# Performance work log

Measured on AMD Instinct MI355X. Metric: run time of the kernel, lower is better.

The kernel has to match this reference:

```python
import jax, jax.numpy as jnp
import numpy as np

B, N, D = 131072, 5, 12   # batch, objects per scene, per-object feature dim
E = 64                    # goal embedding / F1 output dim
H = E // 2                # F1 hidden dim = 32


def setup_inputs() -> dict:
    key = jax.random.key(0)
    ks = jax.random.split(key, 6)
    return {
        "obs": jax.random.normal(ks[0], (B, N, D), dtype=jnp.float32),
        "ghat": jax.random.normal(ks[1], (B, E), dtype=jnp.float32),
        "W1": jax.random.normal(ks[2], (2 * D, H), dtype=jnp.float32) * 0.1,
        "b1": jax.random.normal(ks[3], (H,), dtype=jnp.float32) * 0.1,
        "W2": jax.random.normal(ks[4], (H, E), dtype=jnp.float32) * 0.1,
        "b2": jax.random.normal(ks[5], (E,), dtype=jnp.float32) * 0.1,
    }


def reference(obs, ghat, W1, b1, W2, b2):
    b, n, d = obs.shape
    # all-pairs concat: pairs[i,j,k] = cat(obs[i,j], obs[i,k])  -> [B,N,N,2D]
    o_j = jnp.broadcast_to(obs[:, :, None, :], (b, n, n, d))
    o_k = jnp.broadcast_to(obs[:, None, :, :], (b, n, n, d))
    pairs = jnp.concatenate([o_j, o_k], axis=-1)
    # F1 MLP: Linear -> ReLU -> Linear  -> Z [B,N,N,E]
    Z = jnp.maximum(pairs @ W1 + b1, 0.0) @ W2 + b2
    # attention logits w[i,j,k] = <Z[i,j,k], ghat[i]>; softmax over all N*N pairs
    w = jnp.einsum('bjke,be->bjk', Z, ghat)
    p = jax.nn.softmax(w.reshape(b, -1), axis=1).reshape(b, n, n)
    # z_vector[i,j,k] = sum_e p[i,j,k]*Z[i,j,k,e]; zhat[i,j] = sum_k z_vector
    zhat = jnp.einsum('bjk,bjk->bj', p, Z.sum(axis=-1))  # [B,N]
    # state_rep[i,j] = cat(obs[i,j], ghat[i], zhat[i])  -> [B,N,D+E+N]
    state = jnp.concatenate([
        obs,
        jnp.broadcast_to(ghat[:, None, :], (b, n, E)),
        jnp.broadcast_to(zhat[:, None, :], (b, n, n)),
    ], axis=-1)
    return state.reshape(b, -1)  # Flatten -> [B, N*(D+E+N)] = [B, 405]
```

## Files before the change

### kernel.cpp

```cpp
#include <hip/hip_runtime.h>

#define BLOCK 256
#define NB 5
#define DD 12
#define EE 64
#define HH 32
#define ROW 81
#define OUTW 405
#define TILE 64

__global__ __launch_bounds__(BLOCK) void zhat_kernel(
    const float* __restrict__ obs, const float* __restrict__ ghat,
    const float* __restrict__ W1, const float* __restrict__ b1,
    const float* __restrict__ W2, const float* __restrict__ b2,
    float* __restrict__ zbuf, int zstride, int zoff, int B)
{
    __shared__ float s_w2s[HH];
    __shared__ float s_sb2;
    __shared__ float s_g2[BLOCK * 33];

    const int tid = threadIdx.x;

    if (tid < HH) {
        float s = 0.f;
        #pragma unroll
        for (int e = 0; e < EE; ++e) s += W2[tid * EE + e];
        s_w2s[tid] = s;
    } else if (tid == HH) {
        float s = 0.f;
        #pragma unroll
        for (int e = 0; e < EE; ++e) s += b2[e];
        s_sb2 = s;
    }

    const int i = blockIdx.x * BLOCK + tid;

    float g2[HH];
    #pragma unroll
    for (int h = 0; h < HH; ++h) g2[h] = 0.f;
    if (i < B) {
        const float* grow = ghat + (size_t)i * EE;
        #pragma unroll
        for (int e0 = 0; e0 < EE; e0 += 16) {
            float gc[16];
            const float4* gp = reinterpret_cast<const float4*>(grow + e0);
            #pragma unroll
            for (int q = 0; q < 4; ++q) {
                float4 v = gp[q];
                gc[4*q+0] = v.x; gc[4*q+1] = v.y; gc[4*q+2] = v.z; gc[4*q+3] = v.w;
            }
            #pragma unroll
            for (int h = 0; h < HH; ++h) {
                #pragma unroll
                for (int q = 0; q < 16; ++q)
                    g2[h] += W2[h * EE + e0 + q] * gc[q];
            }
        }
    }
    #pragma unroll
    for (int h = 0; h < HH; ++h) s_g2[tid * 33 + h] = g2[h];
    __syncthreads();

    if (i < B) {
        float o[NB * DD];
        {
            const float4* p = reinterpret_cast<const float4*>(obs + (size_t)i * (NB * DD));
            #pragma unroll
            for (int q = 0; q < NB * DD / 4; ++q) {
                float4 v = p[q];
                o[4*q+0] = v.x; o[4*q+1] = v.y; o[4*q+2] = v.z; o[4*q+3] = v.w;
            }
        }

        float w[NB * NB];
        float hw[NB * NB];
        #pragma unroll
        for (int q = 0; q < NB * NB; ++q) { w[q] = 0.f; hw[q] = 0.f; }

        for (int c = 0; c < HH / 8; ++c) {
            float g2c[8], w2c[8];
            #pragma unroll
            for (int hp = 0; hp < 8; ++hp) {
                g2c[hp] = s_g2[tid * 33 + c * 8 + hp];
                w2c[hp] = s_w2s[c * 8 + hp];
            }
            #pragma unroll
            for (int hp = 0; hp < 8; ++hp) {
                const int h = c * 8 + hp;
                float a[NB], bb[NB];
                #pragma unroll
                for (int j = 0; j < NB; ++j) {
                    float acc = b1[h];
                    float accb = 0.f;
                    #pragma unroll
                    for (int d = 0; d < DD; ++d) {
                        acc  += o[j*DD + d] * W1[d*HH + h];
                        accb += o[j*DD + d] * W1[(DD + d)*HH + h];
                    }
                    a[j] = acc; bb[j] = accb;
                }
                #pragma unroll
                for (int j = 0; j < NB; ++j) {
                    #pragma unroll
                    for (int k = 0; k < NB; ++k) {
                        float hv = fmaxf(a[j] + bb[k], 0.f);
                        w[j*NB + k]  += hv * g2c[hp];
                        hw[j*NB + k] += hv * w2c[hp];
                    }
                }
            }
        }

        float m = w[0];
        #pragma unroll
        for (int q = 1; q < NB * NB; ++q) m = fmaxf(m, w[q]);
        float l = 0.f;
        float zacc[NB], racc[NB];
        #pragma unroll
        for (int j = 0; j < NB; ++j) { zacc[j] = 0.f; racc[j] = 0.f; }
        #pragma unroll
        for (int j = 0; j < NB; ++j) {
            #pragma unroll
            for (int k = 0; k < NB; ++k) {
                float e = __expf(w[j*NB + k] - m);
                l += e;
                zacc[j] += e * hw[j*NB + k];
                racc[j] += e;
            }
        }
        const float invl = 1.f / l;
        const float sb2 = s_sb2;
        float* zr = zbuf + (size_t)i * zstride + zoff;
        #pragma unroll
        for (int j = 0; j < NB; ++j)
            zr[j] = (zacc[j] + sb2 * racc[j]) * invl;
    }
}

__global__ __launch_bounds__(BLOCK) void assemble_kernel(
    const float* __restrict__ obs, const float* __restrict__ ghat,
    const float* __restrict__ zbuf, int zstride, int zoff,
    float* __restrict__ out, int B)
{
    __shared__ float s_obs[TILE * NB * DD];
    __shared__ float s_gh[TILE * EE];
    __shared__ float s_zh[TILE * NB];

    const int tid = threadIdx.x;
    const int r0 = blockIdx.x * TILE;
    const int rows = (B - r0 < TILE) ? (B - r0) : TILE;

    for (int t = tid; t < rows * NB * DD; t += BLOCK)
        s_obs[t] = obs[(size_t)r0 * NB * DD + t];
    for (int t = tid; t < rows * EE; t += BLOCK)
        s_gh[t] = ghat[(size_t)r0 * EE + t];
    for (int t = tid; t < rows * NB; t += BLOCK) {
        const int row = t / NB, k = t - row * NB;
        s_zh[t] = zbuf[(size_t)(r0 + row) * zstride + zoff + k];
    }
    __syncthreads();

    const size_t base = (size_t)r0 * OUTW;
    for (int t = tid; t < rows * OUTW; t += BLOCK) {
        const int il = t / OUTW;
        const int r  = t - il * OUTW;
        const int j  = r / ROW;
        const int rr = r - j * ROW;
        float v;
        if (rr < DD)           v = s_obs[il * NB * DD + j * DD + rr];
        else if (rr < DD + EE) v = s_gh[il * EE + (rr - DD)];
        else                   v = s_zh[il * NB + (rr - (DD + EE))];
        out[base + t] = v;
    }
}

extern "C" void kernel_launch(void* const* d_in, const int* in_sizes, int n_in,
                              void* d_out, int out_size, void* d_ws, size_t ws_size,
                              hipStream_t stream) {
    const float* obs  = (const float*)d_in[0];
    const float* ghat = (const float*)d_in[1];
    const float* W1   = (const float*)d_in[2];
    const float* b1   = (const float*)d_in[3];
    const float* W2   = (const float*)d_in[4];
    const float* b2   = (const float*)d_in[5];
    float* out = (float*)d_out;

    const int B = in_sizes[0] / (NB * DD);

    float* zbuf; int zstride, zoff;
    if (ws_size >= (size_t)B * NB * sizeof(float)) {
        zbuf = (float*)d_ws; zstride = NB;   zoff = 0;
    } else {
        zbuf = out;          zstride = OUTW; zoff = OUTW - NB;
    }

    const int gridA = (B + BLOCK - 1) / BLOCK;
    hipLaunchKernelGGL(zhat_kernel, dim3(gridA), dim3(BLOCK), 0, stream,
                       obs, ghat, W1, b1, W2, b2, zbuf, zstride, zoff, B);

    const int gridB = (B + TILE - 1) / TILE;
    hipLaunchKernelGGL(assemble_kernel, dim3(gridB), dim3(BLOCK), 0, stream,
                       obs, ghat, zbuf, zstride, zoff, out, B);
}
```

Baseline: 146.5 us.

## Split hidden dimension across four threads per row with shuffle reductions

The zhat kernel now assigns four threads to each batch row, with each thread handling 8 of the 32 hidden units. Partial logits and z sums are combined with xor shuffles. This drops the large shared g2 buffer and stages a transposed W1 in shared memory. To save registers, the first-layer hidden activations are recomputed in a second pass after the softmax instead of keeping both accumulator arrays. The aim is more parallelism and occupancy, at the cost of duplicated obs loads and repeated W1 arithmetic. An early return follows the only barrier, so there is no sync hazard.

```diff
diff --git a/kernel.cpp b/kernel.cpp
--- a/kernel.cpp
+++ b/kernel.cpp
@@ -8,6 +8,8 @@
 #define ROW 81
 #define OUTW 405
 #define TILE 64
+#define TPB 4
+#define HPT (HH / TPB)
 
 __global__ __launch_bounds__(BLOCK) void zhat_kernel(
     const float* __restrict__ obs, const float* __restrict__ ghat,
@@ -15,119 +17,171 @@
     const float* __restrict__ W2, const float* __restrict__ b2,
     float* __restrict__ zbuf, int zstride, int zoff, int B)
 {
+    __shared__ float s_W1t[HH * 2 * DD];
     __shared__ float s_w2s[HH];
     __shared__ float s_sb2;
-    __shared__ float s_g2[BLOCK * 33];
 
     const int tid = threadIdx.x;
 
     if (tid < HH) {
         float s = 0.f;
-        #pragma unroll
-        for (int e = 0; e < EE; ++e) s += W2[tid * EE + e];
+        const float4* p = reinterpret_cast<const float4*>(W2 + tid * EE);
+        #pragma unroll
+        for (int q = 0; q < EE / 4; ++q) { float4 v = p[q]; s += (v.x + v.y) + (v.z + v.w); }
         s_w2s[tid] = s;
+        #pragma unroll
+        for (int d = 0; d < 2 * DD; ++d) s_W1t[tid * (2 * DD) + d] = W1[d * HH + tid];
     } else if (tid == HH) {
         float s = 0.f;
         #pragma unroll
         for (int e = 0; e < EE; ++e) s += b2[e];
         s_sb2 = s;
     }
-
-    const int i = blockIdx.x * BLOCK + tid;
-
-    float g2[HH];
-    #pragma unroll
-    for (int h = 0; h < HH; ++h) g2[h] = 0.f;
-    if (i < B) {
-        const float* grow = ghat + (size_t)i * EE;
-        #pragma unroll
-        for (int e0 = 0; e0 < EE; e0 += 16) {
-            float gc[16];
-            const float4* gp = reinterpret_cast<const float4*>(grow + e0);
-            #pragma unroll
-            for (int q = 0; q < 4; ++q) {
-                float4 v = gp[q];
-                gc[4*q+0] = v.x; gc[4*q+1] = v.y; gc[4*q+2] = v.z; gc[4*q+3] = v.w;
-            }
-            #pragma unroll
-            for (int h = 0; h < HH; ++h) {
-                #pragma unroll
-                for (int q = 0; q < 16; ++q)
-                    g2[h] += W2[h * EE + e0 + q] * gc[q];
-            }
-        }
-    }
-    #pragma unroll
-    for (int h = 0; h < HH; ++h) s_g2[tid * 33 + h] = g2[h];
     __syncthreads();
 
-    if (i < B) {
-        float o[NB * DD];
-        {
-            const float4* p = reinterpret_cast<const float4*>(obs + (size_t)i * (NB * DD));
-            #pragma unroll
-            for (int q = 0; q < NB * DD / 4; ++q) {
-                float4 v = p[q];
-                o[4*q+0] = v.x; o[4*q+1] = v.y; o[4*q+2] = v.z; o[4*q+3] = v.w;
-            }
-        }
-
-        float w[NB * NB];
-        float hw[NB * NB];
-        #pragma unroll
-        for (int q = 0; q < NB * NB; ++q) { w[q] = 0.f; hw[q] = 0.f; }
-
-        for (int c = 0; c < HH / 8; ++c) {
-            float g2c[8], w2c[8];
-            #pragma unroll
-            for (int hp = 0; hp < 8; ++hp) {
-                g2c[hp] = s_g2[tid * 33 + c * 8 + hp];
-                w2c[hp] = s_w2s[c * 8 + hp];
-            }
-            #pragma unroll
-            for (int hp = 0; hp < 8; ++hp) {
-                const int h = c * 8 + hp;
-                float a[NB], bb[NB];
-                #pragma unroll
-                for (int j = 0; j < NB; ++j) {
-                    float acc = b1[h];
-                    float accb = 0.f;
-                    #pragma unroll
-                    for (int d = 0; d < DD; ++d) {
-                        acc  += o[j*DD + d] * W1[d*HH + h];
-                        accb += o[j*DD + d] * W1[(DD + d)*HH + h];
-                    }
-                    a[j] = acc; bb[j] = accb;
-                }
-                #pragma unroll
-                for (int j = 0; j < NB; ++j) {
-                    #pragma unroll
-                    for (int k = 0; k < NB; ++k) {
-                        float hv = fmaxf(a[j] + bb[k], 0.f);
-                        w[j*NB + k]  += hv * g2c[hp];
-                        hw[j*NB + k] += hv * w2c[hp];
-                    }
-                }
-            }
-        }
-
-        float m = w[0];
-        #pragma unroll
-        for (int q = 1; q < NB * NB; ++q) m = fmaxf(m, w[q]);
-        float l = 0.f;
-        float zacc[NB], racc[NB];
-        #pragma unroll
-        for (int j = 0; j < NB; ++j) { zacc[j] = 0.f; racc[j] = 0.f; }
+    const int g  = tid & (TPB - 1);
+    const int il = tid >> 2;
+    const int i  = blockIdx.x * (BLOCK / TPB) + il;
+    if (i >= B) return;
+
+    float g2[HPT];
+    #pragma unroll
+    for (int hp = 0; hp < HPT; ++hp) g2[hp] = 0.f;
+    const float* grow = ghat + (size_t)i * EE;
+    #pragma unroll 4
+    for (int ec = 0; ec < EE / 4; ++ec) {
+        const float4 gv = reinterpret_cast<const float4*>(grow)[ec];
+        #pragma unroll
+        for (int hp = 0; hp < HPT; ++hp) {
+            const float4 wv = reinterpret_cast<const float4*>(W2 + (g + TPB * hp) * EE)[ec];
+            g2[hp] += gv.x * wv.x + gv.y * wv.y + gv.z * wv.z + gv.w * wv.w;
+        }
+    }
+
+    float o[NB * DD];
+    {
+        const float4* p = reinterpret_cast<const float4*>(obs + (size_t)i * (NB * DD));
+        #pragma unroll
+        for (int q = 0; q < NB * DD / 4; ++q) {
+            float4 v = p[q];
+            o[4*q+0] = v.x; o[4*q+1] = v.y; o[4*q+2] = v.z; o[4*q+3] = v.w;
+        }
+    }
+
+    float w[NB * NB];
+    #pragma unroll
+    for (int q = 0; q < NB * NB; ++q) w[q] = 0.f;
+
+    #pragma unroll
+    for (int hp = 0; hp < HPT; ++hp) {
+        const int h = g + TPB * hp;
+        float a[NB], bb[NB];
+        const float b1h = b1[h];
+        #pragma unroll
+        for (int j = 0; j < NB; ++j) { a[j] = b1h; bb[j] = 0.f; }
+        const float* w1r = &s_W1t[h * (2 * DD)];
+        #pragma unroll
+        for (int dc = 0; dc < 3; ++dc) {
+            const float4 wv = reinterpret_cast<const float4*>(w1r)[dc];
+            const float wl[4] = {wv.x, wv.y, wv.z, wv.w};
+            #pragma unroll
+            for (int d4 = 0; d4 < 4; ++d4) {
+                const int d = dc * 4 + d4;
+                #pragma unroll
+                for (int j = 0; j < NB; ++j) a[j] += o[j*DD + d] * wl[d4];
+            }
+        }
+        #pragma unroll
+        for (int dc = 0; dc < 3; ++dc) {
+            const float4 wv = reinterpret_cast<const float4*>(w1r + DD)[dc];
+            const float wl[4] = {wv.x, wv.y, wv.z, wv.w};
+            #pragma unroll
+            for (int d4 = 0; d4 < 4; ++d4) {
+                const int d = dc * 4 + d4;
+                #pragma unroll
+                for (int j = 0; j < NB; ++j) bb[j] += o[j*DD + d] * wl[d4];
+            }
+        }
+        const float gv = g2[hp];
+        #pragma unroll
+        for (int j = 0; j < NB; ++j)
+            #pragma unroll
+            for (int k = 0; k < NB; ++k)
+                w[j*NB + k] += fmaxf(a[j] + bb[k], 0.f) * gv;
+    }
+
+    #pragma unroll
+    for (int q = 0; q < NB * NB; ++q) {
+        w[q] += __shfl_xor(w[q], 1);
+        w[q] += __shfl_xor(w[q], 2);
+    }
+
+    float m = w[0];
+    #pragma unroll
+    for (int q = 1; q < NB * NB; ++q) m = fmaxf(m, w[q]);
+    #pragma unroll
+    for (int q = 0; q < NB * NB; ++q) w[q] = __expf(w[q] - m);
+    float l = 0.f;
+    float racc[NB];
+    #pragma unroll
+    for (int j = 0; j < NB; ++j) {
+        float r = 0.f;
+        #pragma unroll
+        for (int k = 0; k < NB; ++k) r += w[j*NB + k];
+        racc[j] = r; l += r;
+    }
+
+    float zacc[NB];
+    #pragma unroll
+    for (int j = 0; j < NB; ++j) zacc[j] = 0.f;
+
+    #pragma unroll
+    for (int hp = 0; hp < HPT; ++hp) {
+        const int h = g + TPB * hp;
+        float a[NB], bb[NB];
+        const float b1h = b1[h];
+        #pragma unroll
+        for (int j = 0; j < NB; ++j) { a[j] = b1h; bb[j] = 0.f; }
+        const float* w1r = &s_W1t[h * (2 * DD)];
+        #pragma unroll
+        for (int dc = 0; dc < 3; ++dc) {
+            const float4 wv = reinterpret_cast<const float4*>(w1r)[dc];
+            const float wl[4] = {wv.x, wv.y, wv.z, wv.w};
+            #pragma unroll
+            for (int d4 = 0; d4 < 4; ++d4) {
+                const int d = dc * 4 + d4;
+                #pragma unroll
+                for (int j = 0; j < NB; ++j) a[j] += o[j*DD + d] * wl[d4];
+            }
+        }
+        #pragma unroll
+        for (int dc = 0; dc < 3; ++dc) {
+            const float4 wv = reinterpret_cast<const float4*>(w1r + DD)[dc];
+            const float wl[4] = {wv.x, wv.y, wv.z, wv.w};
+            #pragma unroll
+            for (int d4 = 0; d4 < 4; ++d4) {
+                const int d = dc * 4 + d4;
+                #pragma unroll
+                for (int j = 0; j < NB; ++j) bb[j] += o[j*DD + d] * wl[d4];
+            }
+        }
+        const float ws = s_w2s[h];
         #pragma unroll
         for (int j = 0; j < NB; ++j) {
-            #pragma unroll
-            for (int k = 0; k < NB; ++k) {
-                float e = __expf(w[j*NB + k] - m);
-                l += e;
-                zacc[j] += e * hw[j*NB + k];
-                racc[j] += e;
-            }
-        }
+            float racc2 = 0.f;
+            #pragma unroll
+            for (int k = 0; k < NB; ++k)
+                racc2 += w[j*NB + k] * fmaxf(a[j] + bb[k], 0.f);
+            zacc[j] += ws * racc2;
+        }
+    }
+
+    #pragma unroll
+    for (int j = 0; j < NB; ++j) {
+        zacc[j] += __shfl_xor(zacc[j], 1);
+        zacc[j] += __shfl_xor(zacc[j], 2);
+    }
+    if (g == 0) {
         const float invl = 1.f / l;
         const float sb2 = s_sb2;
         float* zr = zbuf + (size_t)i * zstride + zoff;
@@ -194,7 +248,7 @@
         zbuf = out;          zstride = OUTW; zoff = OUTW - NB;
     }
 
-    const int gridA = (B + BLOCK - 1) / BLOCK;
+    const int gridA = (B + (BLOCK / TPB) - 1) / (BLOCK / TPB);
     hipLaunchKernelGGL(zhat_kernel, dim3(gridA), dim3(BLOCK), 0, stream,
                        obs, ghat, W1, b1, W2, b2, zbuf, zstride, zoff, B);
 
```

After: 321.5 us. 2.19x slower.

## Split hidden units across thread pairs per row and stage W1 in shared memory

Applied to the files above, without the earlier changes.

Each batch row is now handled by two adjacent lanes, each covering half of the 32 hidden units, and the partial attention logits and weighted sums are combined with an xor shuffle before the softmax. W1 is transposed into shared memory and read with float4 loads, and b1 is staged there too. This doubles the thread count and halves the per-thread register load so latency is hidden better. The cost is redundant ghat@W2 work and redundant obs loads in both lanes, plus the shuffle reduction.

```diff
diff --git a/kernel.cpp b/kernel.cpp
--- a/kernel.cpp
+++ b/kernel.cpp
@@ -8,6 +8,8 @@
 #define ROW 81
 #define OUTW 405
 #define TILE 64
+#define BPB 128
+#define W1P 28
 
 __global__ __launch_bounds__(BLOCK) void zhat_kernel(
     const float* __restrict__ obs, const float* __restrict__ ghat,
@@ -15,16 +17,23 @@
     const float* __restrict__ W2, const float* __restrict__ b2,
     float* __restrict__ zbuf, int zstride, int zoff, int B)
 {
+    __shared__ float s_W1t[HH * W1P];
+    __shared__ float s_b1[HH];
     __shared__ float s_w2s[HH];
     __shared__ float s_sb2;
-    __shared__ float s_g2[BLOCK * 33];
+    __shared__ float s_g2[BLOCK * 17];
 
     const int tid = threadIdx.x;
 
     if (tid < HH) {
+        #pragma unroll
+        for (int d = 0; d < 2 * DD; ++d)
+            s_W1t[tid * W1P + d] = W1[d * HH + tid];
+        s_b1[tid] = b1[tid];
         float s = 0.f;
-        #pragma unroll
-        for (int e = 0; e < EE; ++e) s += W2[tid * EE + e];
+        const float4* p = reinterpret_cast<const float4*>(W2 + tid * EE);
+        #pragma unroll
+        for (int q = 0; q < EE / 4; ++q) { float4 v = p[q]; s += (v.x + v.y) + (v.z + v.w); }
         s_w2s[tid] = s;
     } else if (tid == HH) {
         float s = 0.f;
@@ -33,101 +42,120 @@
         s_sb2 = s;
     }
 
-    const int i = blockIdx.x * BLOCK + tid;
-
-    float g2[HH];
-    #pragma unroll
-    for (int h = 0; h < HH; ++h) g2[h] = 0.f;
-    if (i < B) {
+    const int lane = tid & 63;
+    const int par  = lane & 1;
+    const int slot = (tid >> 6) * 32 + (lane >> 1);
+    int i = blockIdx.x * BPB + slot;
+    const bool valid = (i < B);
+    if (!valid) i = (B > 0) ? B - 1 : 0;
+
+    float o[NB * DD];
+    {
+        const float4* p = reinterpret_cast<const float4*>(obs + (size_t)i * (NB * DD));
+        #pragma unroll
+        for (int q = 0; q < NB * DD / 4; ++q) {
+            float4 v = p[q];
+            o[4*q+0] = v.x; o[4*q+1] = v.y; o[4*q+2] = v.z; o[4*q+3] = v.w;
+        }
+    }
+
+    {
+        float g2[HH];
+        #pragma unroll
+        for (int h = 0; h < HH; ++h) g2[h] = 0.f;
         const float* grow = ghat + (size_t)i * EE;
-        #pragma unroll
-        for (int e0 = 0; e0 < EE; e0 += 16) {
-            float gc[16];
-            const float4* gp = reinterpret_cast<const float4*>(grow + e0);
-            #pragma unroll
-            for (int q = 0; q < 4; ++q) {
-                float4 v = gp[q];
-                gc[4*q+0] = v.x; gc[4*q+1] = v.y; gc[4*q+2] = v.z; gc[4*q+3] = v.w;
+        #pragma unroll 1
+        for (int ec = 0; ec < 8; ++ec) {
+            float gc[8];
+            const float4* gp = reinterpret_cast<const float4*>(grow + ec * 8);
+            float4 v0 = gp[0], v1 = gp[1];
+            gc[0]=v0.x; gc[1]=v0.y; gc[2]=v0.z; gc[3]=v0.w;
+            gc[4]=v1.x; gc[5]=v1.y; gc[6]=v1.z; gc[7]=v1.w;
+            #pragma unroll
+            for (int q = 0; q < 8; ++q) {
+                #pragma unroll
+                for (int h = 0; h < HH; ++h)
+                    g2[h] += gc[q] * W2[h * EE + ec * 8 + q];
             }
-            #pragma unroll
-            for (int h = 0; h < HH; ++h) {
+        }
+        if (par == 0) {
+            #pragma unroll
+            for (int hp = 0; hp < 16; ++hp) s_g2[tid * 17 + hp] = g2[hp];
+        } else {
+            #pragma unroll
+            for (int hp = 0; hp < 16; ++hp) s_g2[tid * 17 + hp] = g2[16 + hp];
+        }
+    }
+    __syncthreads();
+
+    float w[NB * NB], hw[NB * NB];
+    #pragma unroll
+    for (int q = 0; q < NB * NB; ++q) { w[q] = 0.f; hw[q] = 0.f; }
+
+    #pragma unroll 1
+    for (int c = 0; c < 2; ++c) {
+        #pragma unroll
+        for (int hp = 0; hp < 8; ++hp) {
+            const int h = par * 16 + c * 8 + hp;
+            const float g2v = s_g2[tid * 17 + c * 8 + hp];
+            const float w2v = s_w2s[h];
+            const float b1h = s_b1[h];
+            float a[NB], bb[NB];
+            #pragma unroll
+            for (int j = 0; j < NB; ++j) { a[j] = b1h; bb[j] = 0.f; }
+            const float* w1r = &s_W1t[h * W1P];
+            #pragma unroll
+            for (int dc = 0; dc < 3; ++dc) {
+                const float4 wt = *reinterpret_cast<const float4*>(w1r + dc * 4);
+                const float4 wb = *reinterpret_cast<const float4*>(w1r + DD + dc * 4);
+                const float wtl[4] = {wt.x, wt.y, wt.z, wt.w};
+                const float wbl[4] = {wb.x, wb.y, wb.z, wb.w};
                 #pragma unroll
-                for (int q = 0; q < 16; ++q)
-                    g2[h] += W2[h * EE + e0 + q] * gc[q];
-            }
-        }
-    }
-    #pragma unroll
-    for (int h = 0; h < HH; ++h) s_g2[tid * 33 + h] = g2[h];
-    __syncthreads();
-
-    if (i < B) {
-        float o[NB * DD];
-        {
-            const float4* p = reinterpret_cast<const float4*>(obs + (size_t)i * (NB * DD));
-            #pragma unroll
-            for (int q = 0; q < NB * DD / 4; ++q) {
-                float4 v = p[q];
-                o[4*q+0] = v.x; o[4*q+1] = v.y; o[4*q+2] = v.z; o[4*q+3] = v.w;
-            }
-        }
-
-        float w[NB * NB];
-        float hw[NB * NB];
-        #pragma unroll
-        for (int q = 0; q < NB * NB; ++q) { w[q] = 0.f; hw[q] = 0.f; }
-
-        for (int c = 0; c < HH / 8; ++c) {
-            float g2c[8], w2c[8];
-            #pragma unroll
-            for (int hp = 0; hp < 8; ++hp) {
-                g2c[hp] = s_g2[tid * 33 + c * 8 + hp];
-                w2c[hp] = s_w2s[c * 8 + hp];
-            }
-            #pragma unroll
-            for (int hp = 0; hp < 8; ++hp) {
-                const int h = c * 8 + hp;
-                float a[NB], bb[NB];
-                #pragma unroll
-                for (int j = 0; j < NB; ++j) {
-                    float acc = b1[h];
-                    float accb = 0.f;
+                for (int d4 = 0; d4 < 4; ++d4) {
+                    const int d = dc * 4 + d4;
                     #pragma unroll
-                    for (int d = 0; d < DD; ++d) {
-                        acc  += o[j*DD + d] * W1[d*HH + h];
-                        accb += o[j*DD + d] * W1[(DD + d)*HH + h];
-                    }
-                    a[j] = acc; bb[j] = accb;
-                }
-                #pragma unroll
-                for (int j = 0; j < NB; ++j) {
-                    #pragma unroll
-                    for (int k = 0; k < NB; ++k) {
-                        float hv = fmaxf(a[j] + bb[k], 0.f);
-                        w[j*NB + k]  += hv * g2c[hp];
-                        hw[j*NB + k] += hv * w2c[hp];
+                    for (int j = 0; j < NB; ++j) {
+                        a[j]  += o[j*DD + d] * wtl[d4];
+                        bb[j] += o[j*DD + d] * wbl[d4];
                     }
                 }
             }
-        }
-
-        float m = w[0];
-        #pragma unroll
-        for (int q = 1; q < NB * NB; ++q) m = fmaxf(m, w[q]);
-        float l = 0.f;
-        float zacc[NB], racc[NB];
-        #pragma unroll
-        for (int j = 0; j < NB; ++j) { zacc[j] = 0.f; racc[j] = 0.f; }
-        #pragma unroll
-        for (int j = 0; j < NB; ++j) {
-            #pragma unroll
-            for (int k = 0; k < NB; ++k) {
-                float e = __expf(w[j*NB + k] - m);
-                l += e;
-                zacc[j] += e * hw[j*NB + k];
-                racc[j] += e;
+            #pragma unroll
+            for (int j = 0; j < NB; ++j) {
+                #pragma unroll
+                for (int k = 0; k < NB; ++k) {
+                    const float hv = fmaxf(a[j] + bb[k], 0.f);
+                    w[j*NB + k]  += hv * g2v;
+                    hw[j*NB + k] += hv * w2v;
+                }
             }
         }
+    }
+
+    #pragma unroll
+    for (int q = 0; q < NB * NB; ++q) {
+        w[q]  += __shfl_xor(w[q], 1);
+        hw[q] += __shfl_xor(hw[q], 1);
+    }
+
+    float m = w[0];
+    #pragma unroll
+    for (int q = 1; q < NB * NB; ++q) m = fmaxf(m, w[q]);
+    float racc[NB], zacc[NB];
+    float l = 0.f;
+    #pragma unroll
+    for (int j = 0; j < NB; ++j) {
+        float r = 0.f, z = 0.f;
+        #pragma unroll
+        for (int k = 0; k < NB; ++k) {
+            const float e = __expf(w[j*NB + k] - m);
+            r += e;
+            z += e * hw[j*NB + k];
+        }
+        racc[j] = r; zacc[j] = z; l += r;
+    }
+
+    if (valid && par == 0) {
         const float invl = 1.f / l;
         const float sb2 = s_sb2;
         float* zr = zbuf + (size_t)i * zstride + zoff;
@@ -194,7 +222,7 @@
         zbuf = out;          zstride = OUTW; zoff = OUTW - NB;
     }
 
-    const int gridA = (B + BLOCK - 1) / BLOCK;
+    const int gridA = (B + BPB - 1) / BPB;
     hipLaunchKernelGGL(zhat_kernel, dim3(gridA), dim3(BLOCK), 0, stream,
                        obs, ghat, W1, b1, W2, b2, zbuf, zstride, zoff, B);
 
```

New measurement: 145.2 us. No clear change (-0.9%).

## Split each sample across five lanes with shuffles and stage W1 in LDS

Applied to the files above, without the earlier changes.

The zhat kernel now assigns one lane per object (5 lanes per sample, 12 samples per wavefront) instead of one thread per sample. Each lane computes a slice of the ghat·W2 projection and its own row of the pair scores, and exchanges bb terms, g2 values, the max and the softmax sums through wave shuffles. W1 is transposed into shared memory so it can be read with float4 loads, and the large per-thread g2 shared buffer is removed. The aim is to cut register pressure and redundant work per thread and raise occupancy, at the cost of many shuffles and 4 idle lanes per wave.

```diff
diff --git a/kernel.cpp b/kernel.cpp
--- a/kernel.cpp
+++ b/kernel.cpp
@@ -8,6 +8,9 @@
 #define ROW 81
 #define OUTW 405
 #define TILE 64
+#define SPW 12
+#define SPB 48
+#define W1P 28
 
 __global__ __launch_bounds__(BLOCK) void zhat_kernel(
     const float* __restrict__ obs, const float* __restrict__ ghat,
@@ -15,16 +18,24 @@
     const float* __restrict__ W2, const float* __restrict__ b2,
     float* __restrict__ zbuf, int zstride, int zoff, int B)
 {
+    __shared__ float s_W1t[HH * W1P];
+    __shared__ float s_b1[HH];
     __shared__ float s_w2s[HH];
     __shared__ float s_sb2;
-    __shared__ float s_g2[BLOCK * 33];
 
     const int tid = threadIdx.x;
 
+    for (int idx = tid; idx < 2 * DD * HH; idx += BLOCK) {
+        const int h = idx & (HH - 1);
+        const int d = idx >> 5;
+        s_W1t[h * W1P + d] = W1[idx];
+    }
     if (tid < HH) {
+        s_b1[tid] = b1[tid];
         float s = 0.f;
-        #pragma unroll
-        for (int e = 0; e < EE; ++e) s += W2[tid * EE + e];
+        const float4* p = reinterpret_cast<const float4*>(W2 + tid * EE);
+        #pragma unroll
+        for (int q = 0; q < EE / 4; ++q) { float4 v = p[q]; s += (v.x + v.y) + (v.z + v.w); }
         s_w2s[tid] = s;
     } else if (tid == HH) {
         float s = 0.f;
@@ -33,107 +44,107 @@
         s_sb2 = s;
     }
 
-    const int i = blockIdx.x * BLOCK + tid;
-
-    float g2[HH];
-    #pragma unroll
-    for (int h = 0; h < HH; ++h) g2[h] = 0.f;
-    if (i < B) {
-        const float* grow = ghat + (size_t)i * EE;
-        #pragma unroll
-        for (int e0 = 0; e0 < EE; e0 += 16) {
+    const int lane  = tid & 63;
+    const int wv    = tid >> 6;
+    const int sIn   = lane / 5;
+    const int j     = lane - sIn * 5;
+    const int base5 = sIn * 5;
+    const int i     = blockIdx.x * SPB + wv * SPW + sIn;
+    const bool act  = (sIn < SPW) && (i < B);
+    const int ic    = act ? i : (B - 1);
+
+    float o[DD];
+    {
+        const float4* p = reinterpret_cast<const float4*>(obs + (size_t)ic * (NB * DD) + j * DD);
+        #pragma unroll
+        for (int q = 0; q < 3; ++q) {
+            float4 v = p[q];
+            o[4*q+0] = v.x; o[4*q+1] = v.y; o[4*q+2] = v.z; o[4*q+3] = v.w;
+        }
+    }
+
+    float g2own[7];
+    #pragma unroll
+    for (int hp = 0; hp < 7; ++hp) g2own[hp] = 0.f;
+    {
+        const float* grow = ghat + (size_t)ic * EE;
+        #pragma unroll 1
+        for (int ec = 0; ec < 4; ++ec) {
             float gc[16];
-            const float4* gp = reinterpret_cast<const float4*>(grow + e0);
+            const float4* gp = reinterpret_cast<const float4*>(grow + ec * 16);
             #pragma unroll
             for (int q = 0; q < 4; ++q) {
                 float4 v = gp[q];
                 gc[4*q+0] = v.x; gc[4*q+1] = v.y; gc[4*q+2] = v.z; gc[4*q+3] = v.w;
             }
             #pragma unroll
-            for (int h = 0; h < HH; ++h) {
-                #pragma unroll
-                for (int q = 0; q < 16; ++q)
-                    g2[h] += W2[h * EE + e0 + q] * gc[q];
-            }
-        }
-    }
-    #pragma unroll
-    for (int h = 0; h < HH; ++h) s_g2[tid * 33 + h] = g2[h];
-    __syncthreads();
-
-    if (i < B) {
-        float o[NB * DD];
-        {
-            const float4* p = reinterpret_cast<const float4*>(obs + (size_t)i * (NB * DD));
-            #pragma unroll
-            for (int q = 0; q < NB * DD / 4; ++q) {
-                float4 v = p[q];
-                o[4*q+0] = v.x; o[4*q+1] = v.y; o[4*q+2] = v.z; o[4*q+3] = v.w;
-            }
-        }
-
-        float w[NB * NB];
-        float hw[NB * NB];
-        #pragma unroll
-        for (int q = 0; q < NB * NB; ++q) { w[q] = 0.f; hw[q] = 0.f; }
-
-        for (int c = 0; c < HH / 8; ++c) {
-            float g2c[8], w2c[8];
-            #pragma unroll
-            for (int hp = 0; hp < 8; ++hp) {
-                g2c[hp] = s_g2[tid * 33 + c * 8 + hp];
-                w2c[hp] = s_w2s[c * 8 + hp];
-            }
-            #pragma unroll
-            for (int hp = 0; hp < 8; ++hp) {
-                const int h = c * 8 + hp;
-                float a[NB], bb[NB];
-                #pragma unroll
-                for (int j = 0; j < NB; ++j) {
-                    float acc = b1[h];
-                    float accb = 0.f;
+            for (int hp = 0; hp < 7; ++hp) {
+                const int h = j + 5 * hp;
+                if (h < HH) {
+                    const float4* wp = reinterpret_cast<const float4*>(W2 + h * EE + ec * 16);
                     #pragma unroll
-                    for (int d = 0; d < DD; ++d) {
-                        acc  += o[j*DD + d] * W1[d*HH + h];
-                        accb += o[j*DD + d] * W1[(DD + d)*HH + h];
-                    }
-                    a[j] = acc; bb[j] = accb;
-                }
-                #pragma unroll
-                for (int j = 0; j < NB; ++j) {
-                    #pragma unroll
-                    for (int k = 0; k < NB; ++k) {
-                        float hv = fmaxf(a[j] + bb[k], 0.f);
-                        w[j*NB + k]  += hv * g2c[hp];
-                        hw[j*NB + k] += hv * w2c[hp];
+                    for (int qv = 0; qv < 4; ++qv) {
+                        float4 wvv = wp[qv];
+                        const float t = (gc[4*qv+0] * wvv.x + gc[4*qv+1] * wvv.y)
+                                      + (gc[4*qv+2] * wvv.z + gc[4*qv+3] * wvv.w);
+                        g2own[hp] += t;
                     }
                 }
             }
         }
-
-        float m = w[0];
-        #pragma unroll
-        for (int q = 1; q < NB * NB; ++q) m = fmaxf(m, w[q]);
-        float l = 0.f;
-        float zacc[NB], racc[NB];
-        #pragma unroll
-        for (int j = 0; j < NB; ++j) { zacc[j] = 0.f; racc[j] = 0.f; }
-        #pragma unroll
-        for (int j = 0; j < NB; ++j) {
-            #pragma unroll
-            for (int k = 0; k < NB; ++k) {
-                float e = __expf(w[j*NB + k] - m);
-                l += e;
-                zacc[j] += e * hw[j*NB + k];
-                racc[j] += e;
-            }
-        }
-        const float invl = 1.f / l;
+    }
+    __syncthreads();
+
+    float w[NB], hw[NB];
+    #pragma unroll
+    for (int k = 0; k < NB; ++k) { w[k] = 0.f; hw[k] = 0.f; }
+
+    #pragma unroll
+    for (int h = 0; h < HH; ++h) {
+        const float b1h = s_b1[h];
+        const float w2v = s_w2s[h];
+        const float* w1r = &s_W1t[h * W1P];
+        float a = b1h, bb = 0.f;
+        #pragma unroll
+        for (int dc = 0; dc < 3; ++dc) {
+            const float4 wt = *reinterpret_cast<const float4*>(w1r + dc * 4);
+            const float4 wb = *reinterpret_cast<const float4*>(w1r + DD + dc * 4);
+            a  += (o[4*dc+0] * wt.x + o[4*dc+1] * wt.y)
+                + (o[4*dc+2] * wt.z + o[4*dc+3] * wt.w);
+            bb += (o[4*dc+0] * wb.x + o[4*dc+1] * wb.y)
+                + (o[4*dc+2] * wb.z + o[4*dc+3] * wb.w);
+        }
+        const float g2v = __shfl(g2own[h / 5], base5 + (h % 5));
+        #pragma unroll
+        for (int k = 0; k < NB; ++k) {
+            const float bk = __shfl(bb, base5 + k);
+            const float hv = fmaxf(a + bk, 0.f);
+            w[k]  += hv * g2v;
+            hw[k] += hv * w2v;
+        }
+    }
+
+    float mrow = w[0];
+    #pragma unroll
+    for (int k = 1; k < NB; ++k) mrow = fmaxf(mrow, w[k]);
+    float m = mrow;
+    #pragma unroll
+    for (int k = 0; k < NB; ++k) m = fmaxf(m, __shfl(mrow, base5 + k));
+
+    float r = 0.f, z = 0.f;
+    #pragma unroll
+    for (int k = 0; k < NB; ++k) {
+        const float ev = __expf(w[k] - m);
+        r += ev;
+        z += ev * hw[k];
+    }
+    float l = 0.f;
+    #pragma unroll
+    for (int k = 0; k < NB; ++k) l += __shfl(r, base5 + k);
+
+    if (act) {
         const float sb2 = s_sb2;
-        float* zr = zbuf + (size_t)i * zstride + zoff;
-        #pragma unroll
-        for (int j = 0; j < NB; ++j)
-            zr[j] = (zacc[j] + sb2 * racc[j]) * invl;
+        zbuf[(size_t)i * zstride + zoff + j] = (z + sb2 * r) / l;
     }
 }
 
@@ -194,7 +205,7 @@
         zbuf = out;          zstride = OUTW; zoff = OUTW - NB;
     }
 
-    const int gridA = (B + BLOCK - 1) / BLOCK;
+    const int gridA = (B + SPB - 1) / SPB;
     hipLaunchKernelGGL(zhat_kernel, dim3(gridA), dim3(BLOCK), 0, stream,
                        obs, ghat, W1, b1, W2, b2, zbuf, zstride, zoff, B);
 
```

New measurement: 232.0 us. 58.3% more time.
